# Optimization experiments

Measured on AMD Instinct MI355X. Metric: run time of the kernel, lower is better.

## Reference

```python
import jax, jax.numpy as jnp
import numpy as np

C_WEIGHT = 0.005  # 'c' hyperparameter

def _psi(v):
    return jnp.sign(v) * jnp.log1p(jnp.abs(v))

def setup_inputs() -> dict:
    key = jax.random.key(0)
    ks = jax.random.split(key, 16)
    B, P, C = 64, 128, 72
    s = lambda fan_in: 1.0 / np.sqrt(fan_in)
    return {
        'x': jax.random.normal(ks[0], (B, P, 4), dtype=jnp.float32),
        'h': jax.random.normal(ks[1], (B, P, C), dtype=jnp.float32),
        'We1': jax.random.normal(ks[2], (2 * C + 2, 72), dtype=jnp.float32) * s(2 * C + 2),
        'be1': jnp.zeros((72,), dtype=jnp.float32),
        'We2': jax.random.normal(ks[3], (72, 72), dtype=jnp.float32) * s(72),
        'be2': jnp.zeros((72,), dtype=jnp.float32),
        'Wm': jax.random.normal(ks[4], (72, 1), dtype=jnp.float32) * s(72),
        'bm': jnp.zeros((1,), dtype=jnp.float32),
        'Wh1': jax.random.normal(ks[5], (C + 72, 72), dtype=jnp.float32) * s(C + 72),
        'bh1': jnp.zeros((72,), dtype=jnp.float32),
        'Wh2': jax.random.normal(ks[6], (72, 72), dtype=jnp.float32) * s(72),
        'bh2': jnp.zeros((72,), dtype=jnp.float32),
        'Wx': jax.random.normal(ks[7], (72, 1), dtype=jnp.float32) * s(72),
    }

def reference(x, h, We1, be1, We2, be2, Wm, bm, Wh1, bh1, Wh2, bh2, Wx):
    B, P, _ = x.shape
    # pairwise Minkowski invariants: take(...,0)*2 - sum == t^2 - |vec|^2
    x1 = x[:, :, None, :]  # (B,P,1,4)
    x2 = x[:, None, :, :]  # (B,1,P,4)
    d2 = jnp.square(x1 - x2)                      # (B,P,P,4)
    norms = 2.0 * d2[..., 0] - d2.sum(axis=-1)    # (B,P,P)
    z = x1 * x2
    prods = 2.0 * z[..., 0] - z.sum(axis=-1)      # (B,P,P)
    norms = _psi(norms)[..., None]                # use_psi=True
    prods = _psi(prods)[..., None]
    H = h.shape[-1]
    h1 = jnp.broadcast_to(h[:, :, None, :], (B, P, P, H))
    h2 = jnp.broadcast_to(h[:, None, :, :], (B, P, P, H))
    feat = jnp.concatenate([h1, h2, norms, prods], axis=-1)  # (B,P,P,2H+2)
    # phi_e: two Dense+ReLU
    m = jax.nn.relu(feat @ We1 + be1)
    m = jax.nn.relu(m @ We2 + be2)                # (B,P,P,72)
    # phi_m: Dense(1) + sigmoid
    w = jax.nn.sigmoid(m @ Wm + bm)               # (B,P,P,1)
    wm = jnp.sum(w * m, axis=2)                   # (B,P,72)
    # phi_h: Dense+ReLU, Dense; residual add
    g = jax.nn.relu(jnp.concatenate([h, wm], axis=-1) @ Wh1 + bh1)
    dh = g @ Wh2 + bh2
    h_out = h + dh
    # phi_x: Dense(1, no bias); x update
    phi_x = m @ Wx                                # (B,P,P,1)
    x_out = x + C_WEIGHT * jnp.mean(phi_x * x[:, None, :, :], axis=2)
    return (h_out, x_out)
```

## Files before the change

### kernel.cpp

```cpp
#include <hip/hip_runtime.h>
#include <hip/hip_bf16.h>
#include <math.h>

#define B_ 64
#define P_ 128
#define C_ 72
#define PADC 80
#define BCS 88
#define IT 4

typedef __attribute__((ext_vector_type(8))) _Float16 half8v;
typedef __attribute__((ext_vector_type(4))) _Float16 half4v;
typedef __attribute__((ext_vector_type(4))) float f32x4;
typedef __attribute__((ext_vector_type(2))) float f32x2;
typedef __attribute__((ext_vector_type(4))) unsigned int u32x4;

#define FRAG_WE2  0
#define FRAG_WE1A (15 * 64)
#define FRAG_WE1B (30 * 64)
#define FRAG_WH1  (45 * 64)
#define FRAG_WH2  (70 * 64)
#define NFRAG 85

__device__ __forceinline__ float psi_f(float v) {
    float a = fabsf(v);
    return copysignf(__logf(1.0f + a), v);
}
template <int CTRL>
__device__ __forceinline__ float dpp_add(float v) {
    int s = __builtin_amdgcn_update_dpp(0, __builtin_bit_cast(int, v), CTRL, 0xF, 0xF, true);
    return v + __builtin_bit_cast(float, s);
}
__device__ __forceinline__ float red16(float v) {
    v = dpp_add<0xB1>(v);
    v = dpp_add<0x4E>(v);
    v = dpp_add<0x141>(v);
    v = dpp_add<0x140>(v);
    return v;
}
__device__ __forceinline__ half8v cvt8(const float* p) {
    f32x4 a = *(const f32x4*)p;
    f32x4 b = *(const f32x4*)(p + 4);
    half8v r = {(_Float16)a[0], (_Float16)a[1], (_Float16)a[2], (_Float16)a[3],
                (_Float16)b[0], (_Float16)b[1], (_Float16)b[2], (_Float16)b[3]};
    return r;
}

__global__ __launch_bounds__(64) void setup_kernel(
    const float* __restrict__ We1, const float* __restrict__ be1,
    const float* __restrict__ We2, const float* __restrict__ be2,
    const float* __restrict__ Wh1, const float* __restrict__ bh1,
    const float* __restrict__ Wh2, const float* __restrict__ bh2,
    half8v* __restrict__ frags)
{
    const int bid = blockIdx.x;
    const int l = threadIdx.x;
    const int c16 = l & 15, g = l >> 4;

    if (bid >= NFRAG) {
        half4v* tail = (half4v*)(frags + NFRAG * 64);
        const int nt = bid - NFRAG;
        const int n = nt * 16 + c16;
        half4v f = {};
        if (n < C_) {
            #pragma unroll
            for (int jj = 0; jj < 4; ++jj) {
                int k = 64 + 4 * g + jj;
                float w = 0.f;
                if (k < C_) w = We2[k * C_ + n];
                else if (k == C_) w = be2[n];
                f[jj] = (_Float16)w;
            }
        }
        tail[nt * 64 + l] = f;
        return;
    }

    const float* W;
    const float* bias;
    int kmax, rel;
    if (bid < 15)      { W = We2;            bias = be2;     kmax = 72;  rel = bid; }
    else if (bid < 30) { W = We1;            bias = nullptr; kmax = 72;  rel = bid - 15; }
    else if (bid < 45) { W = We1 + 72 * C_;  bias = be1;     kmax = 72;  rel = bid - 30; }
    else if (bid < 70) { W = Wh1;            bias = bh1;     kmax = 144; rel = bid - 45; }
    else               { W = Wh2;            bias = bh2;     kmax = 72;  rel = bid - 70; }
    const int kt = rel / 5, nt = rel - 5 * kt;
    const int n = nt * 16 + c16;

    half8v f = {};
    if (n < C_) {
        #pragma unroll
        for (int jj = 0; jj < 8; ++jj) {
            int k = kt * 32 + g * 8 + jj;
            float w = 0.f;
            if (k < kmax) w = W[k * C_ + n];
            else if (k == kmax && bias) w = bias[n];
            f[jj] = (_Float16)w;
        }
    }
    frags[bid * 64 + l] = f;
}

__global__ __launch_bounds__(64) void pre_kernel(
    const float* __restrict__ h, const half8v* __restrict__ frags,
    _Float16* __restrict__ Ah, _Float16* __restrict__ Bch)
{
    const int l = threadIdx.x, c16 = l & 15, g = l >> 4;
    const int sel = blockIdx.x & 1;
    const int m0 = (blockIdx.x >> 1) * 16;

    const float* hrow = h + (m0 + c16) * C_;
    half8v a0 = cvt8(hrow + g * 8);
    half8v a1 = cvt8(hrow + 32 + g * 8);
    half8v a2 = {};
    if (g == 0) a2 = cvt8(hrow + 64);
    else if (g == 1) a2[0] = (_Float16)1.0f;

    const half8v* F = frags + (sel ? FRAG_WE1B : FRAG_WE1A);
    f32x4 acc[5] = {};
    #pragma unroll
    for (int kt = 0; kt < 3; ++kt) {
        half8v a = (kt == 0) ? a0 : (kt == 1 ? a1 : a2);
        #pragma unroll
        for (int nt = 0; nt < 5; ++nt)
            acc[nt] = __builtin_amdgcn_mfma_f32_16x16x32_f16(a, F[(kt * 5 + nt) * 64 + l], acc[nt], 0, 0, 0);
    }
    _Float16* dst = sel ? Bch : Ah;
    #pragma unroll
    for (int nt = 0; nt < 5; ++nt) {
        int n = nt * 16 + c16;
        if (n < C_) {
            #pragma unroll
            for (int r = 0; r < 4; ++r)
                dst[(m0 + 4 * g + r) * PADC + n] = (_Float16)acc[nt][r];
        }
    }
}

__global__ __launch_bounds__(256, 2) void edge_kernel(
    const float* __restrict__ x, const _Float16* __restrict__ Ah,
    const _Float16* __restrict__ Bch, const float* __restrict__ We1,
    const half8v* __restrict__ frags,
    const float* __restrict__ Wm, const float* __restrict__ bm,
    const float* __restrict__ Wx,
    float* __restrict__ wm_out, float* __restrict__ xacc_out)
{
    __shared__ __align__(16) _Float16 A_s[IT][PADC];
    __shared__ __align__(16) _Float16 Bc_s[P_][BCS];
    __shared__ __align__(16) float xj_s[P_][4];
    __shared__ __align__(16) _Float16 w1_s[PADC], w2_s[PADC];

    const int b  = blockIdx.x >> 5;
    const int it = blockIdx.x & 31;
    const int t  = threadIdx.x;
    const int wv = t >> 6;
    const int l  = t & 63;
    const int c16 = l & 15;
    const int g   = l >> 4;

    {
        const unsigned int* Asrc = (const unsigned int*)(Ah + (b * P_ + it * IT) * PADC);
        for (int idx = t; idx < IT * PADC / 2; idx += 256)
            ((unsigned int*)A_s)[idx] = Asrc[idx];
        for (int cidx = t; cidx < P_ * 10; cidx += 256) {
            int r = cidx / 10, c = cidx - r * 10;
            *(u32x4*)&Bc_s[r][c * 8] = ((const u32x4*)(Bch + (b * P_ + r) * PADC))[c];
        }
        for (int idx = t; idx < P_ * 4; idx += 256)
            ((float*)xj_s)[idx] = x[b * P_ * 4 + idx];
        if (t < 160) {
            int hs = t >= 80;
            int c = t - hs * 80;
            float wv_ = (c < C_) ? We1[(144 + hs) * C_ + c] : 0.f;
            (hs ? w2_s : w1_s)[c] = (_Float16)wv_;
        }
    }
    __syncthreads();

    half8v Wf[2][5];
    #pragma unroll
    for (int kt = 0; kt < 2; ++kt)
        #pragma unroll
        for (int nt = 0; nt < 5; ++nt)
            Wf[kt][nt] = frags[FRAG_WE2 + (kt * 5 + nt) * 64 + l];
    half4v Wf2[5];
    {
        const half4v* tail = (const half4v*)(frags + NFRAG * 64);
        #pragma unroll
        for (int nt = 0; nt < 5; ++nt)
            Wf2[nt] = tail[nt * 64 + l];
    }

    f32x2 WmWx[5][4];
    #pragma unroll
    for (int nt = 0; nt < 5; ++nt)
        #pragma unroll
        for (int r = 0; r < 4; ++r) {
            int ch = nt * 16 + 4 * g + r;
            bool ok = ch < C_;
            WmWx[nt][r][0] = ok ? Wm[ch] : 0.f;
            WmWx[nt][r][1] = ok ? Wx[ch] : 0.f;
        }
    const float bm0 = bm[0];
    const f32x4 zero4 = {0.f, 0.f, 0.f, 0.f};

    const int iloc = wv;
    const int i = it * IT + iloc;
    const int node_i = b * P_ + i;
    const f32x4 xi = *(const f32x4*)&xj_s[i][0];

    f32x4 wmacc[5] = {};
    f32x4 xacc = {0.f, 0.f, 0.f, 0.f};

    #pragma unroll 1
    for (int jt = 0; jt < 8; ++jt) {
        const int j = jt * 16 + c16;
        const f32x4 xjv = *(const f32x4*)&xj_s[j][0];
        float d0 = xi[0] - xjv[0], d1 = xi[1] - xjv[1];
        float d2 = xi[2] - xjv[2], d3 = xi[3] - xjv[3];
        float nn = d0 * d0 - d1 * d1 - d2 * d2 - d3 * d3;
        float pp = xi[0] * xjv[0] - xi[1] * xjv[1] - xi[2] * xjv[2] - xi[3] * xjv[3];
        _Float16 nh = (_Float16)psi_f(nn);
        _Float16 ph = (_Float16)psi_f(pp);
        half8v n8 = {nh, nh, nh, nh, nh, nh, nh, nh};
        half8v p8 = {ph, ph, ph, ph, ph, ph, ph, ph};
        half8v zero8 = {};

        auto chunk = [&](int k) -> half8v {
            half8v v = *(const half8v*)&A_s[iloc][k] + *(const half8v*)&Bc_s[j][k];
            v = __builtin_elementwise_fma(*(const half8v*)&w1_s[k], n8, v);
            v = __builtin_elementwise_fma(*(const half8v*)&w2_s[k], p8, v);
            return __builtin_elementwise_max(v, zero8);
        };
        half8v af0 = chunk(g * 8);
        half8v af1 = chunk(32 + g * 8);

        half4v af2 = {};
        if (g < 2) {
            const int k = 64 + 4 * g;
            half4v n4 = {nh, nh, nh, nh};
            half4v p4 = {ph, ph, ph, ph};
            half4v zero4h = {};
            half4v v = *(const half4v*)&A_s[iloc][k] + *(const half4v*)&Bc_s[j][k];
            v = __builtin_elementwise_fma(*(const half4v*)&w1_s[k], n4, v);
            v = __builtin_elementwise_fma(*(const half4v*)&w2_s[k], p4, v);
            af2 = __builtin_elementwise_max(v, zero4h);
        } else if (g == 2) {
            af2[0] = (_Float16)1.0f;
        }

        f32x4 acc[5] = {};
        #pragma unroll
        for (int nt = 0; nt < 5; ++nt)
            acc[nt] = __builtin_amdgcn_mfma_f32_16x16x32_f16(Wf[0][nt], af0, acc[nt], 0, 0, 0);
        #pragma unroll
        for (int nt = 0; nt < 5; ++nt)
            acc[nt] = __builtin_amdgcn_mfma_f32_16x16x32_f16(Wf[1][nt], af1, acc[nt], 0, 0, 0);
        #pragma unroll
        for (int nt = 0; nt < 5; ++nt)
            acc[nt] = __builtin_amdgcn_mfma_f32_16x16x16f16(Wf2[nt], af2, acc[nt], 0, 0, 0);

        f32x2 wdpd = {0.f, 0.f};
        #pragma unroll
        for (int nt = 0; nt < 5; ++nt) {
            f32x4 m2q = __builtin_elementwise_max(acc[nt], zero4);
            acc[nt] = m2q;
            #pragma unroll
            for (int r = 0; r < 4; ++r) {
                f32x2 vv = {m2q[r], m2q[r]};
                wdpd = __builtin_elementwise_fma(vv, WmWx[nt][r], wdpd);
            }
        }
        {
            f32x2 s;
            s[0] = __shfl_xor(wdpd[0], 16, 64);
            s[1] = __shfl_xor(wdpd[1], 16, 64);
            wdpd += s;
            s[0] = __shfl_xor(wdpd[0], 32, 64);
            s[1] = __shfl_xor(wdpd[1], 32, 64);
            wdpd += s;
        }
        float w_ = __builtin_amdgcn_rcpf(1.f + __expf(-(wdpd[0] + bm0)));
        f32x4 w4 = {w_, w_, w_, w_};
        #pragma unroll
        for (int nt = 0; nt < 5; ++nt)
            wmacc[nt] = __builtin_elementwise_fma(w4, acc[nt], wmacc[nt]);
        f32x4 pd4 = {wdpd[1], wdpd[1], wdpd[1], wdpd[1]};
        xacc = __builtin_elementwise_fma(pd4, xjv, xacc);
    }

    #pragma unroll
    for (int nt = 0; nt < 5; ++nt)
        #pragma unroll
        for (int r = 0; r < 4; ++r)
            wmacc[nt][r] = red16(wmacc[nt][r]);
    #pragma unroll
    for (int q = 0; q < 4; ++q) xacc[q] = red16(xacc[q]);

    if (c16 == 0) {
        #pragma unroll
        for (int nt = 0; nt < 5; ++nt)
            #pragma unroll
            for (int r = 0; r < 4; ++r) {
                int ch = nt * 16 + 4 * g + r;
                if (ch < C_) wm_out[node_i * C_ + ch] = wmacc[nt][r];
            }
    }
    if (l == 0)
        *(f32x4*)&xacc_out[node_i * 4] = xacc;
}

__global__ __launch_bounds__(64) void node_kernel(
    const float* __restrict__ x, const float* __restrict__ h,
    const half8v* __restrict__ frags,
    const float* __restrict__ wm, const float* __restrict__ xacc,
    float* __restrict__ hout, float* __restrict__ xout)
{
    __shared__ _Float16 g_s[16][BCS];
    const int l = threadIdx.x, c16 = l & 15, g = l >> 4;
    const int m0 = blockIdx.x * 16;

    const float* hrow  = h  + (m0 + c16) * C_;
    const float* wmrow = wm + (m0 + c16) * C_;

    half8v a[5];
    #pragma unroll
    for (int kt = 0; kt < 5; ++kt) {
        int k = kt * 32 + g * 8;
        half8v v = {};
        if (k < C_) v = cvt8(hrow + k);
        else if (k < 144) v = cvt8(wmrow + (k - C_));
        else if (k == 144) v[0] = (_Float16)1.0f;
        a[kt] = v;
    }
    f32x4 acc1[5] = {};
    #pragma unroll
    for (int kt = 0; kt < 5; ++kt)
        #pragma unroll
        for (int nt = 0; nt < 5; ++nt)
            acc1[nt] = __builtin_amdgcn_mfma_f32_16x16x32_f16(
                a[kt], frags[FRAG_WH1 + (kt * 5 + nt) * 64 + l], acc1[nt], 0, 0, 0);

    #pragma unroll
    for (int nt = 0; nt < 5; ++nt) {
        int n = nt * 16 + c16;
        #pragma unroll
        for (int r = 0; r < 4; ++r)
            g_s[4 * g + r][n] = (_Float16)fmaxf(acc1[nt][r], 0.f);
    }
    half8v b0 = *(const half8v*)&g_s[c16][g * 8];
    half8v b1 = *(const half8v*)&g_s[c16][32 + g * 8];
    half8v b2 = {};
    if (g == 0) b2 = *(const half8v*)&g_s[c16][64];
    else if (g == 1) b2[0] = (_Float16)1.0f;

    f32x4 acc2[5] = {};
    #pragma unroll
    for (int kt = 0; kt < 3; ++kt) {
        half8v aa = (kt == 0) ? b0 : (kt == 1 ? b1 : b2);
        #pragma unroll
        for (int nt = 0; nt < 5; ++nt)
            acc2[nt] = __builtin_amdgcn_mfma_f32_16x16x32_f16(
                aa, frags[FRAG_WH2 + (kt * 5 + nt) * 64 + l], acc2[nt], 0, 0, 0);
    }
    #pragma unroll
    for (int nt = 0; nt < 5; ++nt) {
        int n = nt * 16 + c16;
        if (n < C_) {
            #pragma unroll
            for (int r = 0; r < 4; ++r) {
                int row = m0 + 4 * g + r;
                hout[row * C_ + n] = h[row * C_ + n] + acc2[nt][r];
            }
        }
    }
    {
        int row = m0 + (l >> 2), d = l & 3;
        xout[row * 4 + d] = x[row * 4 + d] + 0.005f * (xacc[row * 4 + d] * (1.0f / 128.f));
    }
}

extern "C" void kernel_launch(void* const* d_in, const int* in_sizes, int n_in,
                              void* d_out, int out_size, void* d_ws, size_t ws_size,
                              hipStream_t stream) {
    const float* x   = (const float*)d_in[0];
    const float* h   = (const float*)d_in[1];
    const float* We1 = (const float*)d_in[2];
    const float* be1 = (const float*)d_in[3];
    const float* We2 = (const float*)d_in[4];
    const float* be2 = (const float*)d_in[5];
    const float* Wm  = (const float*)d_in[6];
    const float* bm  = (const float*)d_in[7];
    const float* Wh1 = (const float*)d_in[8];
    const float* bh1 = (const float*)d_in[9];
    const float* Wh2 = (const float*)d_in[10];
    const float* bh2 = (const float*)d_in[11];
    const float* Wx  = (const float*)d_in[12];

    const int NNODE = B_ * P_;
    _Float16* Ah  = (_Float16*)d_ws;
    _Float16* Bch = Ah + NNODE * PADC;
    float* wm   = (float*)(Bch + NNODE * PADC);
    float* xacc = wm + NNODE * C_;
    half8v* frags = (half8v*)(xacc + NNODE * 4);

    float* hout = (float*)d_out;
    float* xout = hout + NNODE * C_;

    setup_kernel<<<NFRAG + 5, 64, 0, stream>>>(We1, be1, We2, be2, Wh1, bh1, Wh2, bh2, frags);
    pre_kernel<<<NNODE / 16 * 2, 64, 0, stream>>>(h, frags, Ah, Bch);
    edge_kernel<<<B_ * 32, 256, 0, stream>>>(x, Ah, Bch, We1, frags,
                                             Wm, bm, Wx, wm, xacc);
    node_kernel<<<NNODE / 16, 64, 0, stream>>>(x, h, frags, wm, xacc, hout, xout);
}
```

Before: 64.03 us.

## Pre-swizzle Bc into MFMA fragment layout and drop edge kernel shared memory

The pre kernel now writes the per-node Bc projections in fragment-ordered layout, transposing through a small shared tile, so each lane of the edge kernel loads its operand directly from global memory with coalesced vector loads. The edge kernel drops its shared-memory staging of A, Bc, x and the We1 psi rows along with the block barrier, keeps those values in registers, and prefetches the next j-tile's Bc and x one iteration ahead. This removes per-block LDS fill and synchronisation, which may let more blocks stay resident. The cost is more global/L2 traffic per wave and extra registers, since the four waves of a block each load Bc redundantly. A missing barrier in node_kernel is also added.

```diff
diff --git a/kernel.cpp b/kernel.cpp
--- a/kernel.cpp
+++ b/kernel.cpp
@@ -6,14 +6,12 @@
 #define P_ 128
 #define C_ 72
 #define PADC 80
-#define BCS 88
 #define IT 4
 
 typedef __attribute__((ext_vector_type(8))) _Float16 half8v;
 typedef __attribute__((ext_vector_type(4))) _Float16 half4v;
 typedef __attribute__((ext_vector_type(4))) float f32x4;
 typedef __attribute__((ext_vector_type(2))) float f32x2;
-typedef __attribute__((ext_vector_type(4))) unsigned int u32x4;
 
 #define FRAG_WE2  0
 #define FRAG_WE1A (15 * 64)
@@ -43,6 +41,11 @@
     f32x4 b = *(const f32x4*)(p + 4);
     half8v r = {(_Float16)a[0], (_Float16)a[1], (_Float16)a[2], (_Float16)a[3],
                 (_Float16)b[0], (_Float16)b[1], (_Float16)b[2], (_Float16)b[3]};
+    return r;
+}
+__device__ __forceinline__ half4v cvt4(const float* p) {
+    f32x4 a = *(const f32x4*)p;
+    half4v r = {(_Float16)a[0], (_Float16)a[1], (_Float16)a[2], (_Float16)a[3]};
     return r;
 }
 
@@ -103,8 +106,10 @@
 
 __global__ __launch_bounds__(64) void pre_kernel(
     const float* __restrict__ h, const half8v* __restrict__ frags,
-    _Float16* __restrict__ Ah, _Float16* __restrict__ Bch)
+    _Float16* __restrict__ Ah, half8v* __restrict__ Bcf,
+    half4v* __restrict__ Bcft)
 {
+    __shared__ _Float16 T[16][88];
     const int l = threadIdx.x, c16 = l & 15, g = l >> 4;
     const int sel = blockIdx.x & 1;
     const int m0 = (blockIdx.x >> 1) * 16;
@@ -125,31 +130,51 @@
         for (int nt = 0; nt < 5; ++nt)
             acc[nt] = __builtin_amdgcn_mfma_f32_16x16x32_f16(a, F[(kt * 5 + nt) * 64 + l], acc[nt], 0, 0, 0);
     }
-    _Float16* dst = sel ? Bch : Ah;
-    #pragma unroll
-    for (int nt = 0; nt < 5; ++nt) {
-        int n = nt * 16 + c16;
-        if (n < C_) {
-            #pragma unroll
-            for (int r = 0; r < 4; ++r)
-                dst[(m0 + 4 * g + r) * PADC + n] = (_Float16)acc[nt][r];
-        }
+
+    if (sel == 0) {
+        #pragma unroll
+        for (int nt = 0; nt < 5; ++nt) {
+            int n = nt * 16 + c16;
+            if (n < C_) {
+                #pragma unroll
+                for (int r = 0; r < 4; ++r)
+                    Ah[(m0 + 4 * g + r) * PADC + n] = (_Float16)acc[nt][r];
+            }
+        }
+    } else {
+        #pragma unroll
+        for (int nt = 0; nt < 5; ++nt) {
+            int n = nt * 16 + c16;
+            if (n < C_) {
+                #pragma unroll
+                for (int r = 0; r < 4; ++r)
+                    T[4 * g + r][n] = (_Float16)acc[nt][r];
+            }
+        }
+        {
+            int zr = l >> 2, zc = 72 + (l & 3) * 4;
+            half4v z = {};
+            *(half4v*)&T[zr][zc] = z;
+        }
+        __syncthreads();
+        const int bb = m0 >> 7, jt = (m0 >> 4) & 7;
+        half8v f0 = *(const half8v*)&T[c16][g * 8];
+        half8v f1 = *(const half8v*)&T[c16][32 + g * 8];
+        half4v ft = *(const half4v*)&T[c16][64 + g * 4];
+        Bcf[((bb * 8 + jt) * 2 + 0) * 64 + l] = f0;
+        Bcf[((bb * 8 + jt) * 2 + 1) * 64 + l] = f1;
+        Bcft[(bb * 8 + jt) * 64 + l] = ft;
     }
 }
 
 __global__ __launch_bounds__(256, 2) void edge_kernel(
     const float* __restrict__ x, const _Float16* __restrict__ Ah,
-    const _Float16* __restrict__ Bch, const float* __restrict__ We1,
-    const half8v* __restrict__ frags,
+    const half8v* __restrict__ Bcf, const half4v* __restrict__ Bcft,
+    const float* __restrict__ We1, const half8v* __restrict__ frags,
     const float* __restrict__ Wm, const float* __restrict__ bm,
     const float* __restrict__ Wx,
     float* __restrict__ wm_out, float* __restrict__ xacc_out)
 {
-    __shared__ __align__(16) _Float16 A_s[IT][PADC];
-    __shared__ __align__(16) _Float16 Bc_s[P_][BCS];
-    __shared__ __align__(16) float xj_s[P_][4];
-    __shared__ __align__(16) _Float16 w1_s[PADC], w2_s[PADC];
-
     const int b  = blockIdx.x >> 5;
     const int it = blockIdx.x & 31;
     const int t  = threadIdx.x;
@@ -158,25 +183,6 @@
     const int c16 = l & 15;
     const int g   = l >> 4;
 
-    {
-        const unsigned int* Asrc = (const unsigned int*)(Ah + (b * P_ + it * IT) * PADC);
-        for (int idx = t; idx < IT * PADC / 2; idx += 256)
-            ((unsigned int*)A_s)[idx] = Asrc[idx];
-        for (int cidx = t; cidx < P_ * 10; cidx += 256) {
-            int r = cidx / 10, c = cidx - r * 10;
-            *(u32x4*)&Bc_s[r][c * 8] = ((const u32x4*)(Bch + (b * P_ + r) * PADC))[c];
-        }
-        for (int idx = t; idx < P_ * 4; idx += 256)
-            ((float*)xj_s)[idx] = x[b * P_ * 4 + idx];
-        if (t < 160) {
-            int hs = t >= 80;
-            int c = t - hs * 80;
-            float wv_ = (c < C_) ? We1[(144 + hs) * C_ + c] : 0.f;
-            (hs ? w2_s : w1_s)[c] = (_Float16)wv_;
-        }
-    }
-    __syncthreads();
-
     half8v Wf[2][5];
     #pragma unroll
     for (int kt = 0; kt < 2; ++kt)
@@ -204,18 +210,44 @@
     const float bm0 = bm[0];
     const f32x4 zero4 = {0.f, 0.f, 0.f, 0.f};
 
-    const int iloc = wv;
-    const int i = it * IT + iloc;
+    const float* w1g = We1 + 144 * C_;
+    const float* w2g = We1 + 145 * C_;
+    half8v w1a = cvt8(w1g + g * 8);
+    half8v w1b = cvt8(w1g + 32 + g * 8);
+    half8v w2a = cvt8(w2g + g * 8);
+    half8v w2b = cvt8(w2g + 32 + g * 8);
+    half4v w1t = {}, w2t = {};
+    if (g < 2) { w1t = cvt4(w1g + 64 + g * 4); w2t = cvt4(w2g + 64 + g * 4); }
+
+    const int i = it * IT + wv;
     const int node_i = b * P_ + i;
-    const f32x4 xi = *(const f32x4*)&xj_s[i][0];
+    const f32x4 xi = *(const f32x4*)&x[node_i * 4];
+    const _Float16* Arow = Ah + node_i * PADC;
+    half8v a0 = *(const half8v*)&Arow[g * 8];
+    half8v a1 = *(const half8v*)&Arow[32 + g * 8];
+    half4v at = {};
+    if (g < 2) at = *(const half4v*)&Arow[64 + g * 4];
+
+    const half8v* Bb = Bcf + (size_t)(b * 8) * 2 * 64;
+    const half4v* Bt = Bcft + (size_t)(b * 8) * 64;
+    const float*  xb = x + b * P_ * 4;
+
+    half8v bc0 = Bb[l];
+    half8v bc1 = Bb[64 + l];
+    half4v bct = Bt[l];
+    f32x4 xjv = *(const f32x4*)&xb[c16 * 4];
 
     f32x4 wmacc[5] = {};
     f32x4 xacc = {0.f, 0.f, 0.f, 0.f};
 
     #pragma unroll 1
     for (int jt = 0; jt < 8; ++jt) {
-        const int j = jt * 16 + c16;
-        const f32x4 xjv = *(const f32x4*)&xj_s[j][0];
+        const int njt = (jt + 1) & 7;
+        half8v nbc0 = Bb[(njt * 2) * 64 + l];
+        half8v nbc1 = Bb[(njt * 2 + 1) * 64 + l];
+        half4v nbct = Bt[njt * 64 + l];
+        f32x4 nxjv = *(const f32x4*)&xb[(njt * 16 + c16) * 4];
+
         float d0 = xi[0] - xjv[0], d1 = xi[1] - xjv[1];
         float d2 = xi[2] - xjv[2], d3 = xi[3] - xjv[3];
         float nn = d0 * d0 - d1 * d1 - d2 * d2 - d3 * d3;
@@ -226,24 +258,25 @@
         half8v p8 = {ph, ph, ph, ph, ph, ph, ph, ph};
         half8v zero8 = {};
 
-        auto chunk = [&](int k) -> half8v {
-            half8v v = *(const half8v*)&A_s[iloc][k] + *(const half8v*)&Bc_s[j][k];
-            v = __builtin_elementwise_fma(*(const half8v*)&w1_s[k], n8, v);
-            v = __builtin_elementwise_fma(*(const half8v*)&w2_s[k], p8, v);
-            return __builtin_elementwise_max(v, zero8);
-        };
-        half8v af0 = chunk(g * 8);
-        half8v af1 = chunk(32 + g * 8);
-
+        half8v af0, af1;
+        {
+            half8v v = a0 + bc0;
+            v = __builtin_elementwise_fma(w1a, n8, v);
+            v = __builtin_elementwise_fma(w2a, p8, v);
+            af0 = __builtin_elementwise_max(v, zero8);
+            half8v u = a1 + bc1;
+            u = __builtin_elementwise_fma(w1b, n8, u);
+            u = __builtin_elementwise_fma(w2b, p8, u);
+            af1 = __builtin_elementwise_max(u, zero8);
+        }
         half4v af2 = {};
         if (g < 2) {
-            const int k = 64 + 4 * g;
             half4v n4 = {nh, nh, nh, nh};
             half4v p4 = {ph, ph, ph, ph};
             half4v zero4h = {};
-            half4v v = *(const half4v*)&A_s[iloc][k] + *(const half4v*)&Bc_s[j][k];
-            v = __builtin_elementwise_fma(*(const half4v*)&w1_s[k], n4, v);
-            v = __builtin_elementwise_fma(*(const half4v*)&w2_s[k], p4, v);
+            half4v v = at + bct;
+            v = __builtin_elementwise_fma(w1t, n4, v);
+            v = __builtin_elementwise_fma(w2t, p4, v);
             af2 = __builtin_elementwise_max(v, zero4h);
         } else if (g == 2) {
             af2[0] = (_Float16)1.0f;
@@ -287,6 +320,8 @@
             wmacc[nt] = __builtin_elementwise_fma(w4, acc[nt], wmacc[nt]);
         f32x4 pd4 = {wdpd[1], wdpd[1], wdpd[1], wdpd[1]};
         xacc = __builtin_elementwise_fma(pd4, xjv, xacc);
+
+        bc0 = nbc0; bc1 = nbc1; bct = nbct; xjv = nxjv;
     }
 
     #pragma unroll
@@ -316,7 +351,7 @@
     const float* __restrict__ wm, const float* __restrict__ xacc,
     float* __restrict__ hout, float* __restrict__ xout)
 {
-    __shared__ _Float16 g_s[16][BCS];
+    __shared__ _Float16 g_s[16][88];
     const int l = threadIdx.x, c16 = l & 15, g = l >> 4;
     const int m0 = blockIdx.x * 16;
 
@@ -348,6 +383,7 @@
         for (int r = 0; r < 4; ++r)
             g_s[4 * g + r][n] = (_Float16)fmaxf(acc1[nt][r], 0.f);
     }
+    __syncthreads();
     half8v b0 = *(const half8v*)&g_s[c16][g * 8];
     half8v b1 = *(const half8v*)&g_s[c16][32 + g * 8];
     half8v b2 = {};
@@ -399,17 +435,18 @@
 
     const int NNODE = B_ * P_;
     _Float16* Ah  = (_Float16*)d_ws;
-    _Float16* Bch = Ah + NNODE * PADC;
-    float* wm   = (float*)(Bch + NNODE * PADC);
-    float* xacc = wm + NNODE * C_;
+    half8v* Bcf   = (half8v*)(Ah + NNODE * PADC);
+    half4v* Bcft  = (half4v*)(Bcf + B_ * 8 * 2 * 64);
+    float* wm     = (float*)(Bcft + B_ * 8 * 64);
+    float* xacc   = wm + NNODE * C_;
     half8v* frags = (half8v*)(xacc + NNODE * 4);
 
     float* hout = (float*)d_out;
     float* xout = hout + NNODE * C_;
 
     setup_kernel<<<NFRAG + 5, 64, 0, stream>>>(We1, be1, We2, be2, Wh1, bh1, Wh2, bh2, frags);
-    pre_kernel<<<NNODE / 16 * 2, 64, 0, stream>>>(h, frags, Ah, Bch);
-    edge_kernel<<<B_ * 32, 256, 0, stream>>>(x, Ah, Bch, We1, frags,
+    pre_kernel<<<NNODE / 16 * 2, 64, 0, stream>>>(h, frags, Ah, Bcf, Bcft);
+    edge_kernel<<<B_ * 32, 256, 0, stream>>>(x, Ah, Bcf, Bcft, We1, frags,
                                              Wm, bm, Wx, wm, xacc);
     node_kernel<<<NNODE / 16, 64, 0, stream>>>(x, h, frags, wm, xacc, hout, xout);
 }
```

Result: faster. 60.30 us (-5.8%).
